# Kernel optimization log

Hardware: AMD Instinct MI355X
Metric: run time of the kernel (lower is better)

## Reference

```python
import jax, jax.numpy as jnp
import numpy as np

K = 32          # neighbors
HEAD_DIM = 8    # out_channels // num_heads = 64 // 8


def _ln(x, g, b, eps=1e-5):
    m = x.mean(-1, keepdims=True)
    v = ((x - m) ** 2).mean(-1, keepdims=True)
    return (x - m) * jax.lax.rsqrt(v + eps) * g + b


def _knn(x, k):
    # x: [B,N,3]; torch code takes top-k of NEGATIVE squared distance -> nearest
    sq = jnp.sum(x * x, axis=-1)                        # [B,N]
    inner = jnp.einsum('bnc,bmc->bnm', x, x)            # [B,N,N]
    neg_dist = -(sq[:, :, None] - 2.0 * inner + sq[:, None, :])
    return jax.lax.top_k(neg_dist, k)[1]                # [B,N,k]


def _gather(points, idx):
    # points: [B,M,C], idx: [B,N,K] -> [B,N,K,C]
    return jax.vmap(lambda p, i: p[i])(points, idx)


def _forward(xyz, features, ln1_g, ln1_b, Wq, bq, Wk, bk, Wv, bv,
             d_W1, d_b1, d_g, d_b, d_W2, d_b2,
             g_W1, g_b1, g_g, g_b, g_W2, g_b2,
             Wo, bo, ln2_g, ln2_b, ca_W1, ca_b1, ca_W2, ca_b2, ln3_g, ln3_b):
    fn = _ln(features, ln1_g, ln1_b)                    # norm1
    idx = _knn(xyz, K)                                  # [B,N,K]
    nxyz = _gather(xyz, idx)                            # [B,N,K,3]
    nfeat = _gather(fn, idx)                            # [B,N,K,C]
    pos_diff = xyz[:, :, None, :] - nxyz                # [B,N,K,3]
    # fc_delta: Linear -> LN -> ReLU -> Linear
    pe = jax.nn.relu(_ln(pos_diff @ d_W1 + d_b1, d_g, d_b)) @ d_W2 + d_b2
    q = (fn @ Wq + bq)[:, :, None, :]                   # [B,N,1,C]
    k = nfeat @ Wk + bk                                 # [B,N,K,C]
    v = nfeat @ Wv + bv
    # head permutes in torch are identity reshapes; vector attention in [B,N,K,C]
    attn_in = q - k + pe
    a = jax.nn.relu(_ln(attn_in @ g_W1 + g_b1, g_g, g_b)) @ g_W2 + g_b2
    a = jax.nn.softmax(a / np.sqrt(HEAD_DIM).astype(np.float32), axis=2)
    out = jnp.sum(a * (v + pe), axis=2)                 # [B,N,C]
    out = _ln(out @ Wo + bo, ln2_g, ln2_b)              # fc_out + norm2
    cw = jax.nn.sigmoid(jax.nn.relu(out.mean(axis=1) @ ca_W1 + ca_b1) @ ca_W2 + ca_b2)
    out = _ln(out * cw[:, None, :], ln3_g, ln3_b)       # channel attn + norm3
    return out + features                               # in==out -> no skip_proj


def setup_inputs() -> dict:
    key = jax.random.key(0)
    ks = jax.random.split(key, 12)
    B, N, C = 2, 8192, 64
    s = 1.0 / np.sqrt(C)
    w = lambda k, shape, sc: jax.random.normal(k, shape, jnp.float32) * sc
    return dict(
        xyz=jax.random.normal(ks[0], (B, N, 3), jnp.float32),
        features=jax.random.normal(ks[1], (B, N, C), jnp.float32),
        ln1_g=jnp.ones(C), ln1_b=jnp.zeros(C),
        Wq=w(ks[2], (C, C), s), bq=jnp.zeros(C),
        Wk=w(ks[3], (C, C), s), bk=jnp.zeros(C),
        Wv=w(ks[4], (C, C), s), bv=jnp.zeros(C),
        d_W1=w(ks[5], (3, C), 1.0 / np.sqrt(3)), d_b1=jnp.zeros(C),
        d_g=jnp.ones(C), d_b=jnp.zeros(C),
        d_W2=w(ks[6], (C, C), s), d_b2=jnp.zeros(C),
        g_W1=w(ks[7], (C, C), s), g_b1=jnp.zeros(C),
        g_g=jnp.ones(C), g_b=jnp.zeros(C),
        g_W2=w(ks[8], (C, C), s), g_b2=jnp.zeros(C),
        Wo=w(ks[9], (C, C), s), bo=jnp.zeros(C),
        ln2_g=jnp.ones(C), ln2_b=jnp.zeros(C),
        ca_W1=w(ks[10], (C, C // 4), s), ca_b1=jnp.zeros(C // 4),
        ca_W2=w(ks[11], (C // 4, C), 1.0 / np.sqrt(C // 4)), ca_b2=jnp.zeros(C),
        ln3_g=jnp.ones(C), ln3_b=jnp.zeros(C),
    )


def reference(xyz, features, ln1_g, ln1_b, Wq, bq, Wk, bk, Wv, bv,
              d_W1, d_b1, d_g, d_b, d_W2, d_b2,
              g_W1, g_b1, g_g, g_b, g_W2, g_b2,
              Wo, bo, ln2_g, ln2_b, ca_W1, ca_b1, ca_W2, ca_b2, ln3_g, ln3_b):
    return _forward(xyz, features, ln1_g, ln1_b, Wq, bq, Wk, bk, Wv, bv,
                    d_W1, d_b1, d_g, d_b, d_W2, d_b2,
                    g_W1, g_b1, g_g, g_b, g_W2, g_b2,
                    Wo, bo, ln2_g, ln2_b, ca_W1, ca_b1, ca_W2, ca_b2, ln3_g, ln3_b)
```

## Files before the change

kernel.cpp:

```cpp
#include <hip/hip_runtime.h>

static constexpr int gB = 2;
static constexpr int gN = 8192;
static constexpr int gC = 64;
static constexpr int gK = 32;

using u16 = unsigned short;
using u32 = unsigned int;
using u64 = unsigned long long;

__device__ __forceinline__ float wsum(float v) {
#pragma unroll
    for (int m = 32; m; m >>= 1) v += __shfl_xor(v, m, 64);
    return v;
}

__device__ __forceinline__ u16 f2bf(float f) {
    u32 u = __float_as_uint(f);
    return (u16)((u + 0x7FFFu + ((u >> 16) & 1u)) >> 16);
}
__device__ __forceinline__ float bf2f(u16 v) {
    return __uint_as_float(((u32)v) << 16);
}

__global__ __launch_bounds__(256) void k_lnqkv(
    const float* __restrict__ feat, const float* __restrict__ ln1g, const float* __restrict__ ln1b,
    const float* __restrict__ Wq, const float* __restrict__ bq,
    const float* __restrict__ Wk, const float* __restrict__ bk,
    const float* __restrict__ Wv, const float* __restrict__ bv,
    float* __restrict__ Qo, float* __restrict__ Ko, float* __restrict__ Vo,
    float* __restrict__ zero_region)
{
    if (blockIdx.x == 0) zero_region[threadIdx.x] = 0.f;
    int wave = threadIdx.x >> 6, lane = threadIdx.x & 63;
    int p = blockIdx.x * 4 + wave;
    float x = feat[(size_t)p * gC + lane];
    float mu = wsum(x) * (1.f / 64);
    float d = x - mu;
    float var = wsum(d * d) * (1.f / 64);
    float inv = 1.f / sqrtf(var + 1e-5f);
    float fn = d * inv * ln1g[lane] + ln1b[lane];
    float qa = bq[lane], ka = bk[lane], va = bv[lane];
    for (int cp = 0; cp < 64; ++cp) {
        float hv = __shfl(fn, cp, 64);
        qa += hv * Wq[cp * 64 + lane];
        ka += hv * Wk[cp * 64 + lane];
        va += hv * Wv[cp * 64 + lane];
    }
    size_t o = (size_t)p * gC + lane;
    Qo[o] = qa; Ko[o] = ka; Vo[o] = va;
}

__global__ __launch_bounds__(256) void k_pack(const float* __restrict__ xyz,
                                              float4* __restrict__ pk4)
{
#pragma clang fp contract(off)
    int p = blockIdx.x * 256 + threadIdx.x;
    const float* s = xyz + (size_t)p * 3;
    float x = s[0], y = s[1], z = s[2];
    float n = sqrtf((x * x + y * y) + z * z);
    pk4[p] = make_float4(x, y, z, n * n);
}

__global__ __launch_bounds__(256) void k_knn(const float4* __restrict__ pk4, int* __restrict__ idxo)
{
#pragma clang fp contract(off)
    __shared__ float xs[1024], ys[1024], zs[1024], ws[1024];
    int tid = threadIdx.x;
    int wave = tid >> 6, lane = tid & 63;
    int q = blockIdx.x * 4 + wave;
    int b = q >> 13;
    int n = q & (gN - 1);
    const float4* base = pk4 + (size_t)b * gN;
    float4 me = base[n];
    float xi = me.x, yi = me.y, zi = me.z;
    float sqi = me.w;
    u64 lst[10];
#pragma unroll
    for (int e = 0; e < 10; ++e) lst[e] = 0ull;

    for (int tile = 0; tile < 8; ++tile) {
        __syncthreads();
#pragma unroll
        for (int t0 = 0; t0 < 4; ++t0) {
            int t = tid + (t0 << 8);
            float4 c = base[(tile << 10) + t];
            xs[t] = c.x; ys[t] = c.y; zs[t] = c.z; ws[t] = c.w;
        }
        __syncthreads();
#pragma unroll 4
        for (int i = 0; i < 16; ++i) {
            int t = (i << 6) | lane;
            int j = (tile << 10) + t;
            float inner = (xi * xs[t] + yi * ys[t]) + zi * zs[t];
            float nd = -((sqi - 2.0f * inner) + ws[t]);
            u32 u = __float_as_uint(nd);
            u32 kh = u ^ (0x80000000u | (u32)((int)u >> 31));
            u64 pk = ((u64)kh << 32) | (u32)(8191 - j);
            if (pk > lst[9]) {
                lst[9] = pk;
#pragma unroll
                for (int e = 9; e > 0; --e) {
                    if (lst[e] > lst[e - 1]) { u64 tm = lst[e - 1]; lst[e - 1] = lst[e]; lst[e] = tm; }
                }
            }
        }
    }
    int* op = idxo + (size_t)q * gK;
    for (int r = 0; r < gK; ++r) {
        u64 g = lst[0];
#pragma unroll
        for (int m = 32; m; m >>= 1) {
            u64 o = __shfl_xor(g, m, 64);
            g = (o > g) ? o : g;
        }
        if (lst[0] == g) {
#pragma unroll
            for (int e = 0; e < 9; ++e) lst[e] = lst[e + 1];
            lst[9] = 0ull;
        }
        if (lane == 0) op[r] = 8191 - (int)(g & 0x1FFFu);
    }
}

__global__ __launch_bounds__(256, 2) void k_attn(
    const float* __restrict__ xyz,
    const float* __restrict__ Qb, const float* __restrict__ Kb, const float* __restrict__ Vb,
    const int* __restrict__ idxi,
    const float* __restrict__ dW1, const float* __restrict__ db1,
    const float* __restrict__ dgv, const float* __restrict__ dbv,
    const float* __restrict__ dW2, const float* __restrict__ db2,
    const float* __restrict__ gW1, const float* __restrict__ gb1,
    const float* __restrict__ ggv, const float* __restrict__ gbv,
    const float* __restrict__ gW2, const float* __restrict__ gb2,
    float* __restrict__ att)
{
    __shared__ u16 wd2s[64 * 64];
    __shared__ u16 wg1s[64 * 64];
    __shared__ u16 wg2s[64 * 64];
    __shared__ float hbuf[4][32][64];
    __shared__ u16 pebuf[4][32][64];
    __shared__ float4 dxb[4][32];
    __shared__ int jb[4][32];

    int tid = threadIdx.x;
    int w = tid >> 6, lane = tid & 63;
    int p = blockIdx.x * 4 + w;
    int b = p >> 13;

    for (int i = tid; i < 4096; i += 256) {
        int cp = i >> 6, c = i & 63;
        int di = c * 64 + ((((cp >> 2) ^ (c & 15)) << 2) | (cp & 3));
        wd2s[di] = f2bf(dW2[i]);
        wg1s[di] = f2bf(gW1[i]);
        wg2s[di] = f2bf(gW2[i]);
    }
    if (lane < 32) {
        int j = idxi[(size_t)p * gK + lane];
        jb[w][lane] = j;
        const float* xp = xyz + (size_t)p * 3;
        const float* xj = xyz + ((size_t)b * gN + j) * 3;
        dxb[w][lane] = make_float4(xp[0] - xj[0], xp[1] - xj[1], xp[2] - xj[2], 0.f);
    }
    __syncthreads();

    float w1x = dW1[lane], w1y = dW1[64 + lane], w1z = dW1[128 + lane], vb1 = db1[lane];
    float vdg = dgv[lane], vdb = dbv[lane];
    float vb2 = db2[lane];
    float vg1b = gb1[lane], vgg = ggv[lane], vgb = gbv[lane], vg2b = gb2[lane];
    float q = Qb[(size_t)p * gC + lane];

#pragma unroll
    for (int kk = 0; kk < 32; ++kk) {
        float4 d4 = dxb[w][kk];
        float t = d4.x * w1x + d4.y * w1y + d4.z * w1z + vb1;
        float mu = wsum(t) * (1.f / 64);
        float td = t - mu;
        float var = wsum(td * td) * (1.f / 64);
        float inv = 1.f / sqrtf(var + 1e-5f);
        hbuf[w][kk][lane] = fmaxf(td * inv * vdg + vdb, 0.f);
    }

    float acc[32];

#pragma unroll
    for (int kk = 0; kk < 32; ++kk) acc[kk] = vb2;
    for (int cp4 = 0; cp4 < 16; ++cp4) {
        int pg = cp4 ^ (lane & 15);
        uint2 wp = *reinterpret_cast<const uint2*>(&wd2s[lane * 64 + pg * 4]);
        float w0 = bf2f((u16)(wp.x & 0xFFFFu)), w1 = bf2f((u16)(wp.x >> 16));
        float w2 = bf2f((u16)(wp.y & 0xFFFFu)), w3 = bf2f((u16)(wp.y >> 16));
#pragma unroll
        for (int kk = 0; kk < 32; ++kk) {
            float4 h4 = *reinterpret_cast<const float4*>(&hbuf[w][kk][cp4 * 4]);
            acc[kk] += h4.x * w0 + h4.y * w1 + h4.z * w2 + h4.w * w3;
        }
    }
#pragma unroll
    for (int kk = 0; kk < 32; ++kk) pebuf[w][kk][lane] = f2bf(acc[kk]);

    {
        const float* Kbb = Kb + (size_t)b * gN * gC;
#pragma unroll
        for (int kk = 0; kk < 32; ++kk) {
            float kv = Kbb[(size_t)jb[w][kk] * gC + lane];
            hbuf[w][kk][lane] = (q - kv) + acc[kk];
        }
    }

#pragma unroll
    for (int kk = 0; kk < 32; ++kk) acc[kk] = vg1b;
    for (int cp4 = 0; cp4 < 16; ++cp4) {
        int pg = cp4 ^ (lane & 15);
        uint2 wp = *reinterpret_cast<const uint2*>(&wg1s[lane * 64 + pg * 4]);
        float w0 = bf2f((u16)(wp.x & 0xFFFFu)), w1 = bf2f((u16)(wp.x >> 16));
        float w2 = bf2f((u16)(wp.y & 0xFFFFu)), w3 = bf2f((u16)(wp.y >> 16));
#pragma unroll
        for (int kk = 0; kk < 32; ++kk) {
            float4 h4 = *reinterpret_cast<const float4*>(&hbuf[w][kk][cp4 * 4]);
            acc[kk] += h4.x * w0 + h4.y * w1 + h4.z * w2 + h4.w * w3;
        }
    }
#pragma unroll
    for (int kk = 0; kk < 32; ++kk) {
        float a = acc[kk];
        float mu = wsum(a) * (1.f / 64);
        float ad = a - mu;
        float var = wsum(ad * ad) * (1.f / 64);
        float inv = 1.f / sqrtf(var + 1e-5f);
        hbuf[w][kk][lane] = fmaxf(ad * inv * vgg + vgb, 0.f);
    }

#pragma unroll
    for (int kk = 0; kk < 32; ++kk) acc[kk] = vg2b;
    for (int cp4 = 0; cp4 < 16; ++cp4) {
        int pg = cp4 ^ (lane & 15);
        uint2 wp = *reinterpret_cast<const uint2*>(&wg2s[lane * 64 + pg * 4]);
        float w0 = bf2f((u16)(wp.x & 0xFFFFu)), w1 = bf2f((u16)(wp.x >> 16));
        float w2 = bf2f((u16)(wp.y & 0xFFFFu)), w3 = bf2f((u16)(wp.y >> 16));
#pragma unroll
        for (int kk = 0; kk < 32; ++kk) {
            float4 h4 = *reinterpret_cast<const float4*>(&hbuf[w][kk][cp4 * 4]);
            acc[kk] += h4.x * w0 + h4.y * w1 + h4.z * w2 + h4.w * w3;
        }
    }

#pragma unroll
    for (int kk = 0; kk < 32; ++kk) acc[kk] *= 0.3535533905932738f;
    float mx = acc[0];
#pragma unroll
    for (int kk = 1; kk < 32; ++kk) mx = fmaxf(mx, acc[kk]);
    float s = 0.f;
#pragma unroll
    for (int kk = 0; kk < 32; ++kk) { acc[kk] = expf(acc[kk] - mx); s += acc[kk]; }
    {
        const float* Vbb = Vb + (size_t)b * gN * gC;
        float o = 0.f;
#pragma unroll
        for (int kk = 0; kk < 32; ++kk) {
            float vv = Vbb[(size_t)jb[w][kk] * gC + lane];
            o += acc[kk] * (vv + bf2f(pebuf[w][kk][lane]));
        }
        att[(size_t)p * gC + lane] = o / s;
    }
}

__global__ __launch_bounds__(256) void k_out(
    float* __restrict__ att,
    const float* __restrict__ Wo, const float* __restrict__ bo,
    const float* __restrict__ ln2g, const float* __restrict__ ln2b,
    float* __restrict__ meanb)
{
    __shared__ __align__(16) float hb[4][64];
    int lane = threadIdx.x & 63;
    int p = blockIdx.x * 4 + (threadIdx.x >> 6);
    int b = p >> 13;
    float* hbuf = hb[threadIdx.x >> 6];
    float wo[64];
#pragma unroll
    for (int r = 0; r < 64; ++r) wo[r] = Wo[r * 64 + lane];
    float x = att[(size_t)p * gC + lane];
    hbuf[lane] = x;
    float acc = bo[lane];
#pragma unroll
    for (int q4 = 0; q4 < 16; ++q4) {
        float4 hq = *reinterpret_cast<const float4*>(&hbuf[q4 * 4]);
        acc += hq.x * wo[q4 * 4 + 0] + hq.y * wo[q4 * 4 + 1]
             + hq.z * wo[q4 * 4 + 2] + hq.w * wo[q4 * 4 + 3];
    }
    float mu = wsum(acc) * (1.f / 64);
    float d = acc - mu;
    float var = wsum(d * d) * (1.f / 64);
    float inv = 1.f / sqrtf(var + 1e-5f);
    float y = d * inv * ln2g[lane] + ln2b[lane];
    att[(size_t)p * gC + lane] = y;
    atomicAdd(&meanb[b * 64 + lane], y * (1.f / gN));
}

__global__ void k_cw(const float* __restrict__ meanb,
                     const float* __restrict__ caW1, const float* __restrict__ cab1,
                     const float* __restrict__ caW2, const float* __restrict__ cab2,
                     float* __restrict__ cw)
{
    int b = blockIdx.x, lane = threadIdx.x;
    float mv = meanb[b * 64 + lane];
    float hj = (lane < 16) ? cab1[lane] : 0.f;
    for (int cp = 0; cp < 64; ++cp) {
        float mcp = __shfl(mv, cp, 64);
        if (lane < 16) hj += mcp * caW1[cp * 16 + lane];
    }
    hj = fmaxf(hj, 0.f);
    float acc = cab2[lane];
    for (int jj = 0; jj < 16; ++jj) {
        float hv = __shfl(hj, jj, 64);
        acc += hv * caW2[jj * 64 + lane];
    }
    cw[b * 64 + lane] = 1.f / (1.f + expf(-acc));
}

__global__ __launch_bounds__(256) void k_final(
    const float* __restrict__ out2, const float* __restrict__ cw,
    const float* __restrict__ ln3g, const float* __restrict__ ln3b,
    const float* __restrict__ feat, float* __restrict__ outp)
{
    int lane = threadIdx.x & 63;
    int p = blockIdx.x * 4 + (threadIdx.x >> 6);
    int b = p >> 13;
    float x = out2[(size_t)p * gC + lane] * cw[b * 64 + lane];
    float mu = wsum(x) * (1.f / 64);
    float d = x - mu;
    float var = wsum(d * d) * (1.f / 64);
    float inv = 1.f / sqrtf(var + 1e-5f);
    float y = d * inv * ln3g[lane] + ln3b[lane];
    outp[(size_t)p * gC + lane] = y + feat[(size_t)p * gC + lane];
}

extern "C" void kernel_launch(void* const* d_in, const int* in_sizes, int n_in,
                              void* d_out, int out_size, void* d_ws, size_t ws_size,
                              hipStream_t stream)
{
    (void)in_sizes; (void)n_in; (void)out_size; (void)ws_size;
    const float* xyz  = (const float*)d_in[0];
    const float* feat = (const float*)d_in[1];
    const float* ln1g = (const float*)d_in[2];
    const float* ln1b = (const float*)d_in[3];
    const float* Wq   = (const float*)d_in[4];
    const float* bq   = (const float*)d_in[5];
    const float* Wk   = (const float*)d_in[6];
    const float* bk   = (const float*)d_in[7];
    const float* Wv   = (const float*)d_in[8];
    const float* bv   = (const float*)d_in[9];
    const float* dW1  = (const float*)d_in[10];
    const float* db1  = (const float*)d_in[11];
    const float* dg   = (const float*)d_in[12];
    const float* db   = (const float*)d_in[13];
    const float* dW2  = (const float*)d_in[14];
    const float* db2  = (const float*)d_in[15];
    const float* gW1  = (const float*)d_in[16];
    const float* gb1  = (const float*)d_in[17];
    const float* gg   = (const float*)d_in[18];
    const float* gb   = (const float*)d_in[19];
    const float* gW2  = (const float*)d_in[20];
    const float* gb2  = (const float*)d_in[21];
    const float* Wo   = (const float*)d_in[22];
    const float* bo   = (const float*)d_in[23];
    const float* ln2g = (const float*)d_in[24];
    const float* ln2b = (const float*)d_in[25];
    const float* caW1 = (const float*)d_in[26];
    const float* cab1 = (const float*)d_in[27];
    const float* caW2 = (const float*)d_in[28];
    const float* cab2 = (const float*)d_in[29];
    const float* ln3g = (const float*)d_in[30];
    const float* ln3b = (const float*)d_in[31];

    const size_t BNC = (size_t)gB * gN * gC;
    float* Q    = (float*)d_ws;
    float* Kt   = Q + BNC;
    float* Vt   = Kt + BNC;
    float* att  = Vt + BNC;
    int*   idx  = (int*)(att + BNC);
    float* meanb = (float*)(idx + (size_t)gB * gN * gK);
    float* cw    = meanb + 128;
    float4* pk4  = (float4*)(cw + 128);

    const int PB = (gB * gN) / 4;

    k_lnqkv<<<PB, 256, 0, stream>>>(feat, ln1g, ln1b, Wq, bq, Wk, bk, Wv, bv, Q, Kt, Vt, meanb);
    k_pack<<<(gB * gN) / 256, 256, 0, stream>>>(xyz, pk4);
    k_knn<<<PB, 256, 0, stream>>>(pk4, idx);
    k_attn<<<PB, 256, 0, stream>>>(xyz, Q, Kt, Vt, idx,
                                   dW1, db1, dg, db, dW2, db2,
                                   gW1, gb1, gg, gb, gW2, gb2, att);
    k_out<<<PB, 256, 0, stream>>>(att, Wo, bo, ln2g, ln2b, meanb);
    k_cw<<<gB, 64, 0, stream>>>(meanb, caW1, cab1, caW2, cab2, cw);
    k_final<<<PB, 256, 0, stream>>>(att, cw, ln3g, ln3b, feat, (float*)d_out);
}
```

Baseline: 1.054 ms.

## Fuse xyz packing into LN/QKV, fold channel-attention into final, prefilter kNN insertions

Packs xyz into float4 inside the LN/QKV kernel and removes the separate pack kernel. The channel-attention weight computation moves into the final kernel, so every wave recomputes the tiny MLP instead of launching a separate kernel. The kNN loop gains a cheap 32-bit threshold check against the current 10th-best key before building the 64-bit packed key and running the insertion. Together these cut two launches and some per-candidate work, at the cost of redundant MLP work per wave in k_final.

```diff
diff --git a/kernel.cpp b/kernel.cpp
--- a/kernel.cpp
+++ b/kernel.cpp
@@ -29,11 +29,19 @@
     const float* __restrict__ Wk, const float* __restrict__ bk,
     const float* __restrict__ Wv, const float* __restrict__ bv,
     float* __restrict__ Qo, float* __restrict__ Ko, float* __restrict__ Vo,
-    float* __restrict__ zero_region)
+    float* __restrict__ zero_region,
+    const float* __restrict__ xyz, float4* __restrict__ pk4)
 {
     if (blockIdx.x == 0) zero_region[threadIdx.x] = 0.f;
     int wave = threadIdx.x >> 6, lane = threadIdx.x & 63;
     int p = blockIdx.x * 4 + wave;
+    if (lane == 0) {
+#pragma clang fp contract(off)
+        const float* s = xyz + (size_t)p * 3;
+        float x = s[0], y = s[1], z = s[2];
+        float nn = sqrtf((x * x + y * y) + z * z);
+        pk4[p] = make_float4(x, y, z, nn * nn);
+    }
     float x = feat[(size_t)p * gC + lane];
     float mu = wsum(x) * (1.f / 64);
     float d = x - mu;
@@ -51,17 +59,6 @@
     Qo[o] = qa; Ko[o] = ka; Vo[o] = va;
 }
 
-__global__ __launch_bounds__(256) void k_pack(const float* __restrict__ xyz,
-                                              float4* __restrict__ pk4)
-{
-#pragma clang fp contract(off)
-    int p = blockIdx.x * 256 + threadIdx.x;
-    const float* s = xyz + (size_t)p * 3;
-    float x = s[0], y = s[1], z = s[2];
-    float n = sqrtf((x * x + y * y) + z * z);
-    pk4[p] = make_float4(x, y, z, n * n);
-}
-
 __global__ __launch_bounds__(256) void k_knn(const float4* __restrict__ pk4, int* __restrict__ idxo)
 {
 #pragma clang fp contract(off)
@@ -78,6 +75,7 @@
     u64 lst[10];
 #pragma unroll
     for (int e = 0; e < 10; ++e) lst[e] = 0ull;
+    u32 khmin = 0u;
 
     for (int tile = 0; tile < 8; ++tile) {
         __syncthreads();
@@ -91,17 +89,20 @@
 #pragma unroll 4
         for (int i = 0; i < 16; ++i) {
             int t = (i << 6) | lane;
-            int j = (tile << 10) + t;
             float inner = (xi * xs[t] + yi * ys[t]) + zi * zs[t];
             float nd = -((sqi - 2.0f * inner) + ws[t]);
             u32 u = __float_as_uint(nd);
             u32 kh = u ^ (0x80000000u | (u32)((int)u >> 31));
-            u64 pk = ((u64)kh << 32) | (u32)(8191 - j);
-            if (pk > lst[9]) {
-                lst[9] = pk;
-#pragma unroll
-                for (int e = 9; e > 0; --e) {
-                    if (lst[e] > lst[e - 1]) { u64 tm = lst[e - 1]; lst[e - 1] = lst[e]; lst[e] = tm; }
+            if (kh >= khmin) {
+                int j = (tile << 10) + t;
+                u64 pk = ((u64)kh << 32) | (u32)(8191 - j);
+                if (pk > lst[9]) {
+                    lst[9] = pk;
+#pragma unroll
+                    for (int e = 9; e > 0; --e) {
+                        if (lst[e] > lst[e - 1]) { u64 tm = lst[e - 1]; lst[e - 1] = lst[e]; lst[e] = tm; }
+                    }
+                    khmin = (u32)(lst[9] >> 32);
                 }
             }
         }
@@ -297,12 +298,17 @@
     atomicAdd(&meanb[b * 64 + lane], y * (1.f / gN));
 }
 
-__global__ void k_cw(const float* __restrict__ meanb,
-                     const float* __restrict__ caW1, const float* __restrict__ cab1,
-                     const float* __restrict__ caW2, const float* __restrict__ cab2,
-                     float* __restrict__ cw)
-{
-    int b = blockIdx.x, lane = threadIdx.x;
+__global__ __launch_bounds__(256) void k_final(
+    const float* __restrict__ out2, const float* __restrict__ meanb,
+    const float* __restrict__ caW1, const float* __restrict__ cab1,
+    const float* __restrict__ caW2, const float* __restrict__ cab2,
+    const float* __restrict__ ln3g, const float* __restrict__ ln3b,
+    const float* __restrict__ feat, float* __restrict__ outp)
+{
+    int lane = threadIdx.x & 63;
+    int p = blockIdx.x * 4 + (threadIdx.x >> 6);
+    int b = p >> 13;
+
     float mv = meanb[b * 64 + lane];
     float hj = (lane < 16) ? cab1[lane] : 0.f;
     for (int cp = 0; cp < 64; ++cp) {
@@ -310,23 +316,14 @@
         if (lane < 16) hj += mcp * caW1[cp * 16 + lane];
     }
     hj = fmaxf(hj, 0.f);
-    float acc = cab2[lane];
+    float accw = cab2[lane];
     for (int jj = 0; jj < 16; ++jj) {
         float hv = __shfl(hj, jj, 64);
-        acc += hv * caW2[jj * 64 + lane];
-    }
-    cw[b * 64 + lane] = 1.f / (1.f + expf(-acc));
-}
-
-__global__ __launch_bounds__(256) void k_final(
-    const float* __restrict__ out2, const float* __restrict__ cw,
-    const float* __restrict__ ln3g, const float* __restrict__ ln3b,
-    const float* __restrict__ feat, float* __restrict__ outp)
-{
-    int lane = threadIdx.x & 63;
-    int p = blockIdx.x * 4 + (threadIdx.x >> 6);
-    int b = p >> 13;
-    float x = out2[(size_t)p * gC + lane] * cw[b * 64 + lane];
+        accw += hv * caW2[jj * 64 + lane];
+    }
+    float cwv = 1.f / (1.f + expf(-accw));
+
+    float x = out2[(size_t)p * gC + lane] * cwv;
     float mu = wsum(x) * (1.f / 64);
     float d = x - mu;
     float var = wsum(d * d) * (1.f / 64);
@@ -380,18 +377,17 @@
     float* att  = Vt + BNC;
     int*   idx  = (int*)(att + BNC);
     float* meanb = (float*)(idx + (size_t)gB * gN * gK);
-    float* cw    = meanb + 128;
-    float4* pk4  = (float4*)(cw + 128);
+    float4* pk4  = (float4*)(meanb + 256);
 
     const int PB = (gB * gN) / 4;
 
-    k_lnqkv<<<PB, 256, 0, stream>>>(feat, ln1g, ln1b, Wq, bq, Wk, bk, Wv, bv, Q, Kt, Vt, meanb);
-    k_pack<<<(gB * gN) / 256, 256, 0, stream>>>(xyz, pk4);
+    k_lnqkv<<<PB, 256, 0, stream>>>(feat, ln1g, ln1b, Wq, bq, Wk, bk, Wv, bv,
+                                    Q, Kt, Vt, meanb, xyz, pk4);
     k_knn<<<PB, 256, 0, stream>>>(pk4, idx);
     k_attn<<<PB, 256, 0, stream>>>(xyz, Q, Kt, Vt, idx,
                                    dW1, db1, dg, db, dW2, db2,
                                    gW1, gb1, gg, gb, gW2, gb2, att);
     k_out<<<PB, 256, 0, stream>>>(att, Wo, bo, ln2g, ln2b, meanb);
-    k_cw<<<gB, 64, 0, stream>>>(meanb, caW1, cab1, caW2, cab2, cw);
-    k_final<<<PB, 256, 0, stream>>>(att, cw, ln3g, ln3b, feat, (float*)d_out);
-}
+    k_final<<<PB, 256, 0, stream>>>(att, meanb, caW1, cab1, caW2, cab2,
+                                    ln3g, ln3b, feat, (float*)d_out);
+}
```

Measured after the change: 1.109 ms. 5.2% more time.
